# Kernel tuning notes

Measured on AMD Instinct MI355X. Metric: run time of the kernel, lower is better.

## Reference

```python
import math
import jax, jax.numpy as jnp
import numpy as np

D_MODEL = 768
EXPAND = 2
D_INNER = EXPAND * D_MODEL  # 1536
D_STATE = 16
D_CONV = 4
DT_RANK = math.ceil(D_INNER / 16)  # 96
B, L = 2, 2048
LN_EPS = 1e-5


def setup_inputs() -> dict:
    key = jax.random.key(0)
    ks = jax.random.split(key, 10)
    x = jax.random.normal(ks[0], (B, L, D_MODEL), dtype=jnp.float32)
    ln_g = jnp.ones((D_MODEL,), jnp.float32)
    ln_b = jnp.zeros((D_MODEL,), jnp.float32)
    W_in = jax.random.normal(ks[1], (D_MODEL, 2 * D_INNER), jnp.float32) / np.sqrt(D_MODEL)
    conv_w = jax.random.normal(ks[2], (D_INNER, 1, D_CONV), jnp.float32) / np.sqrt(D_CONV)
    conv_b = jax.random.normal(ks[3], (D_INNER,), jnp.float32) * 0.02
    W_xproj = jax.random.normal(ks[4], (D_INNER, DT_RANK + 2 * D_STATE), jnp.float32) / np.sqrt(D_INNER)
    W_dt = jax.random.normal(ks[5], (DT_RANK, D_INNER), jnp.float32) / np.sqrt(DT_RANK)
    # dt bias init: inverse-softplus of dt ~ LogUniform(1e-3, 1e-1)
    dt = jnp.exp(jax.random.uniform(ks[6], (D_INNER,)) * (math.log(0.1) - math.log(0.001)) + math.log(0.001))
    b_dt = dt + jnp.log(-jnp.expm1(-dt))
    log_A = jnp.log(jnp.tile(jnp.arange(1, D_STATE + 1, dtype=jnp.float32), (D_INNER, 1)))  # (d_inner, N)
    D_param = jnp.ones((D_INNER,), jnp.float32)
    W_out = jax.random.normal(ks[7], (D_INNER, D_MODEL), jnp.float32) / np.sqrt(D_INNER)
    return dict(x=x, ln_g=ln_g, ln_b=ln_b, W_in=W_in, conv_w=conv_w, conv_b=conv_b,
                W_xproj=W_xproj, W_dt=W_dt, b_dt=b_dt, log_A=log_A, D_param=D_param, W_out=W_out)


def _mamba_block(x, ln_g, ln_b, W_in, conv_w, conv_b, W_xproj, W_dt, b_dt, log_A, D_param, W_out):
    residual = x
    # LayerNorm
    mu = jnp.mean(x, axis=-1, keepdims=True)
    var = jnp.var(x, axis=-1, keepdims=True)
    xn = (x - mu) * jax.lax.rsqrt(var + LN_EPS) * ln_g + ln_b
    # in projection -> (u, v)
    uv = xn @ W_in  # (B, L, 2*d_inner)
    u, v = jnp.split(uv, 2, axis=-1)
    # causal depthwise conv1d along length (torch pads both sides then truncates -> left pad only)
    u_c = jnp.transpose(u, (0, 2, 1))  # (B, d_inner, L)
    u_c = jax.lax.conv_general_dilated(
        u_c, conv_w, window_strides=(1,), padding=[(D_CONV - 1, 0)],
        dimension_numbers=('NCH', 'OIH', 'NCH'), feature_group_count=D_INNER)
    u_c = u_c + conv_b[None, :, None]
    u = jnp.transpose(u_c, (0, 2, 1))  # (B, L, d_inner)
    u = jax.nn.silu(u)
    # Selective SSM
    x_dbl = u @ W_xproj  # (B, L, dt_rank + 2N)
    dlt, Bm, Cm = jnp.split(x_dbl, [DT_RANK, DT_RANK + D_STATE], axis=-1)
    delta = jax.nn.softplus(dlt @ W_dt + b_dt)  # (B, L, d_inner)
    A = -jnp.exp(log_A)  # (d_inner, N)
    A_bar = jnp.exp(jnp.einsum('bld,dn->bldn', delta, A))         # discretized A
    Bu = jnp.einsum('bld,bln,bld->bldn', delta, Bm, u)            # B_bar * u
    # parallel scan: h_k = A_bar_k * h_{k-1} + Bu_k
    def comb(e1, e2):
        a1, b1 = e1
        a2, b2 = e2
        return a1 * a2, a2 * b1 + b2
    _, h = jax.lax.associative_scan(comb, (A_bar, Bu), axis=1)
    y = jnp.einsum('bldn,bln->bld', h, Cm) + u * D_param
    # gate + residual
    y = y * jax.nn.silu(v)
    return y @ W_out + residual


def reference(x, ln_g, ln_b, W_in, conv_w, conv_b, W_xproj, W_dt, b_dt, log_A, D_param, W_out):
    return _mamba_block(x, ln_g, ln_b, W_in, conv_w, conv_b, W_xproj, W_dt, b_dt, log_A, D_param, W_out)
```

## Files before the change

### kernel.cpp

```cpp
#include <hip/hip_runtime.h>

#define D_MODEL 768
#define D_INNER 1536
#define D_STATE 16
#define DT_RANK 96
#define BB 2
#define LL 2048
#define TT (BB*LL)
#define NC 64
#define CL 32
#define SKK 4
#define LOG2E 1.44269504f

typedef unsigned short u16;
typedef short bf16x8 __attribute__((ext_vector_type(8)));
typedef unsigned short u16x8 __attribute__((ext_vector_type(8)));
typedef float f32x4  __attribute__((ext_vector_type(4)));

__device__ __forceinline__ float bf2f(u16 u) {
    union { unsigned int i; float f; } c; c.i = ((unsigned int)u) << 16; return c.f;
}
__device__ __forceinline__ u16 f2bf(float f) {
    union { float f; unsigned int i; } c; c.f = f;
    unsigned int x = c.i;
    return (u16)((x + 0x7fffu + ((x >> 16) & 1u)) >> 16);
}
__device__ __forceinline__ float bfu_lo(unsigned int u) {
    union { unsigned int i; float f; } c; c.i = u << 16; return c.f;
}
__device__ __forceinline__ float bfu_hi(unsigned int u) {
    union { unsigned int i; float f; } c; c.i = u & 0xFFFF0000u; return c.f;
}
__device__ __forceinline__ float ldx(const void* p, size_t i, bool f32) {
    return f32 ? ((const float*)p)[i] : bf2f(((const u16*)p)[i]);
}

__device__ __forceinline__ void gload16(const u16* g, u16* l) {
    __builtin_amdgcn_global_load_lds(
        (const __attribute__((address_space(1))) unsigned int*)g,
        (__attribute__((address_space(3))) unsigned int*)l, 16, 0, 0);
}

__device__ __forceinline__ void xcd_swz(int& bx, int& by) {
    const int gx = gridDim.x;
    const int cpx = (gx * gridDim.y) >> 3;
    const int bid = by * gx + bx;
    const int w = (bid & 7) * cpx + (bid >> 3);
    bx = w % gx; by = w / gx;
}

__global__ void detect_kernel(const void* x, int* flag)
{
    __shared__ int bad;
    if (threadIdx.x == 0) bad = 0;
    __syncthreads();
    const u16* p = (const u16*)x;
    int local = 0;
    for (int i = threadIdx.x; i < 2048; i += 256) {
        const float v = bf2f(p[2 * i]);
        if (!(fabsf(v) < 1e4f)) local = 1;
    }
    if (local) atomicOr(&bad, 1);
    __syncthreads();
    if (threadIdx.x == 0) *flag = bad;
}

__global__ __launch_bounds__(256) void transpose_all_kernel(
    const void* __restrict__ W_in, const void* __restrict__ W_xp,
    const void* __restrict__ W_dt, const void* __restrict__ W_out,
    u16* __restrict__ WtIn, u16* __restrict__ WtXp,
    u16* __restrict__ WtDt, u16* __restrict__ WtOut,
    const int* __restrict__ flagp)
{
    const bool f32 = (*flagp != 0);
    int bid = blockIdx.x;
    const void* src; u16* dst; int K, N, bx, by;
    if (bid < 576)      { src = W_in;  dst = WtIn;  K = 768;  N = 3072; bx = bid % 48; by = bid / 48; }
    else if (bid < 624) { bid -= 576; src = W_xp;  dst = WtXp;  K = 1536; N = 128;  bx = bid % 2;  by = bid / 2; }
    else if (bid < 672) { bid -= 624; src = W_dt;  dst = WtDt;  K = 96;   N = 1536; bx = bid % 24; by = bid / 24; }
    else                { bid -= 672; src = W_out; dst = WtOut; K = 1536; N = 768;  bx = bid % 12; by = bid / 12; }
    __shared__ u16 tile[64][72];
    const int t  = threadIdx.x;
    const int n0 = bx * 64, k0 = by * 64;
    {
        const int r = t >> 2, c = (t & 3) * 16;
        const int k = k0 + r;
        if (k < K) {
            #pragma unroll
            for (int i = 0; i < 16; ++i)
                tile[r][c + i] = f2bf(ldx(src, (size_t)k * N + n0 + c + i, f32));
        }
    }
    __syncthreads();
    {
        const int nl = t >> 2, kl = (t & 3) * 16;
        const int n = n0 + nl;
        #pragma unroll
        for (int i = 0; i < 16; ++i) {
            const int k = k0 + kl + i;
            if (k < K) dst[(size_t)n * K + k] = tile[kl + i][nl];
        }
    }
}

__global__ __launch_bounds__(256) void ln_kernel(const void* __restrict__ x,
    const void* __restrict__ g, const void* __restrict__ b, u16* __restrict__ xn,
    const int* __restrict__ flagp)
{
    const bool f32 = (*flagp != 0);
    const int tok = blockIdx.x;
    const int tid = threadIdx.x;
    const size_t base = (size_t)tok * D_MODEL;
    float v[3];
    v[0] = ldx(x, base + tid, f32);
    v[1] = ldx(x, base + tid + 256, f32);
    v[2] = ldx(x, base + tid + 512, f32);
    float s = v[0] + v[1] + v[2];
    float q = v[0]*v[0] + v[1]*v[1] + v[2]*v[2];
    #pragma unroll
    for (int o = 32; o > 0; o >>= 1) {
        s += __shfl_down(s, o, 64);
        q += __shfl_down(q, o, 64);
    }
    __shared__ float ss[4], qq[4];
    if ((tid & 63) == 0) { ss[tid >> 6] = s; qq[tid >> 6] = q; }
    __syncthreads();
    const float S = ss[0] + ss[1] + ss[2] + ss[3];
    const float Q = qq[0] + qq[1] + qq[2] + qq[3];
    const float mu  = S * (1.f / D_MODEL);
    const float var = Q * (1.f / D_MODEL) - mu * mu;
    const float rs  = rsqrtf(var + 1e-5f);
    u16* outr = xn + base;
    #pragma unroll
    for (int i = 0; i < 3; ++i) {
        const int c = tid + i * 256;
        outr[c] = f2bf((v[i] - mu) * rs * ldx(g, c, f32) + ldx(b, c, f32));
    }
}

template<int EPI>
__global__ __launch_bounds__(256) void mfma_gemm(
    const u16* __restrict__ A, const u16* __restrict__ Bt,
    u16* __restrict__ C, void* __restrict__ Cout, const void* __restrict__ aux,
    float* __restrict__ Cf, const int* __restrict__ flagp,
    int Kslice, int lda, int ldbt, int ldc)
{
    const bool f32 = (*flagp != 0);
    __shared__ alignas(16) u16 As[2 * 64 * 32];
    __shared__ alignas(16) u16 Bs[2 * 64 * 32];
    const int tid  = threadIdx.x;
    const int wave = tid >> 6, lane = tid & 63;
    const int lrow = lane & 15, quad = lane >> 4;
    int bx = blockIdx.x, by = blockIdx.y;
    if (gridDim.z == 1) xcd_swz(bx, by);
    const int row0 = by * 64, col0 = bx * 64;
    const int k0   = blockIdx.z * Kslice;
    const int srow = wave * 16 + (lane >> 2);
    const int skk  = (lane & 3) * 8;
    const int wb   = wave * 512;
    const u16* gA = A  + (size_t)(row0 + srow) * lda  + k0 + skk;
    const u16* gB = Bt + (size_t)(col0 + srow) * ldbt + k0 + skk;
    const int nst = Kslice >> 5;
    gload16(gA, &As[wb]);
    gload16(gB, &Bs[wb]);
    f32x4 acc[4] = {{0.f,0.f,0.f,0.f},{0.f,0.f,0.f,0.f},{0.f,0.f,0.f,0.f},{0.f,0.f,0.f,0.f}};
    int cur = 0;
    for (int t = 0; t < nst; ++t) {
        __syncthreads();
        const int boff = cur << 11;
        if (t + 1 < nst) {
            const int poff = boff ^ 2048;
            gload16(gA + (t + 1) * 32, &As[poff + wb]);
            gload16(gB + (t + 1) * 32, &Bs[poff + wb]);
        }
        const bf16x8 af = *(const bf16x8*)(&As[boff + (wave * 16 + lrow) * 32 + quad * 8]);
        #pragma unroll
        for (int q = 0; q < 4; ++q) {
            const bf16x8 bq = *(const bf16x8*)(&Bs[boff + (q * 16 + lrow) * 32 + quad * 8]);
            acc[q] = __builtin_amdgcn_mfma_f32_16x16x32_bf16(af, bq, acc[q], 0, 0, 0);
        }
        cur ^= 1;
    }
    #pragma unroll
    for (int t = 0; t < 4; ++t) {
        #pragma unroll
        for (int r = 0; r < 4; ++r) {
            const int row = row0 + wave * 16 + quad * 4 + r;
            const int col = col0 + t * 16 + lrow;
            const size_t idx = (size_t)row * ldc + col;
            float vv = acc[t][r];
            if (EPI == 1) {
                vv += ldx(aux, col, f32);
                vv = (vv > 20.f) ? vv : log1pf(__expf(vv));
                C[idx] = f2bf(vv);
            } else if (EPI == 2) {
                vv += ldx(aux, idx, f32);
                if (f32) ((float*)Cout)[idx] = vv;
                else     ((u16*)Cout)[idx]   = f2bf(vv);
            } else if (EPI == 3) {
                atomicAdd(&Cf[idx], vv);
            } else {
                C[idx] = f2bf(vv);
            }
        }
    }
}

template<int EPI>
__global__ __launch_bounds__(256) void mfma_gemm128(
    const u16* __restrict__ A, const u16* __restrict__ Bt,
    u16* __restrict__ C, void* __restrict__ Cout, const void* __restrict__ aux,
    const int* __restrict__ flagp,
    int K, int lda, int ldbt, int ldc)
{
    const bool f32 = (*flagp != 0);
    __shared__ alignas(16) u16 As[2 * 128 * 32];
    __shared__ alignas(16) u16 Bs[2 * 128 * 32];
    const int tid  = threadIdx.x;
    const int wave = tid >> 6, lane = tid & 63;
    const int lrow = lane & 15, quad = lane >> 4;
    const int wy = wave >> 1, wx = wave & 1;
    int bx = blockIdx.x, by = blockIdx.y;
    if (gridDim.z == 1) xcd_swz(bx, by);
    const int row0 = by * 128, col0 = bx * 128;
    const int skk = (lane & 3) * 8;
    const int r0 = wave * 16 + (lane >> 2);
    const int r1 = r0 + 64;
    const int wb0 = wave * 512, wb1 = (wave + 4) * 512;
    const u16* gA0 = A  + (size_t)(row0 + r0) * lda  + skk;
    const u16* gA1 = A  + (size_t)(row0 + r1) * lda  + skk;
    const u16* gB0 = Bt + (size_t)(col0 + r0) * ldbt + skk;
    const u16* gB1 = Bt + (size_t)(col0 + r1) * ldbt + skk;
    const int nst = K >> 5;
    gload16(gA0, &As[wb0]);
    gload16(gA1, &As[wb1]);
    gload16(gB0, &Bs[wb0]);
    gload16(gB1, &Bs[wb1]);
    f32x4 acc[4][4];
    #pragma unroll
    for (int i = 0; i < 4; ++i)
        #pragma unroll
        for (int j = 0; j < 4; ++j) acc[i][j] = (f32x4){0.f,0.f,0.f,0.f};
    int cur = 0;
    for (int t = 0; t < nst; ++t) {
        __syncthreads();
        const int boff = cur << 12;
        if (t + 1 < nst) {
            const int poff = boff ^ 4096;
            const int kt = (t + 1) * 32;
            gload16(gA0 + kt, &As[poff + wb0]);
            gload16(gA1 + kt, &As[poff + wb1]);
            gload16(gB0 + kt, &Bs[poff + wb0]);
            gload16(gB1 + kt, &Bs[poff + wb1]);
        }
        bf16x8 af[4], bf_[4];
        #pragma unroll
        for (int i = 0; i < 4; ++i)
            af[i] = *(const bf16x8*)(&As[boff + (wy * 64 + i * 16 + lrow) * 32 + quad * 8]);
        #pragma unroll
        for (int j = 0; j < 4; ++j)
            bf_[j] = *(const bf16x8*)(&Bs[boff + (wx * 64 + j * 16 + lrow) * 32 + quad * 8]);
        #pragma unroll
        for (int i = 0; i < 4; ++i)
            #pragma unroll
            for (int j = 0; j < 4; ++j)
                acc[i][j] = __builtin_amdgcn_mfma_f32_16x16x32_bf16(af[i], bf_[j], acc[i][j], 0, 0, 0);
        cur ^= 1;
    }
    #pragma unroll
    for (int i = 0; i < 4; ++i) {
        #pragma unroll
        for (int j = 0; j < 4; ++j) {
            #pragma unroll
            for (int r = 0; r < 4; ++r) {
                const int row = row0 + wy * 64 + i * 16 + quad * 4 + r;
                const int col = col0 + wx * 64 + j * 16 + lrow;
                const size_t idx = (size_t)row * ldc + col;
                float vv = acc[i][j][r];
                if (EPI == 1) {
                    vv += ldx(aux, col, f32);
                    vv = (vv > 20.f) ? vv : log1pf(__expf(vv));
                    C[idx] = f2bf(vv);
                } else if (EPI == 2) {
                    vv += ldx(aux, idx, f32);
                    if (f32) ((float*)Cout)[idx] = vv;
                    else     ((u16*)Cout)[idx]   = f2bf(vv);
                } else {
                    C[idx] = f2bf(vv);
                }
            }
        }
    }
}

__global__ __launch_bounds__(256) void convert_kernel(const float* __restrict__ src,
                                                      u16* __restrict__ dst, int n)
{
    const int i = blockIdx.x * 256 + threadIdx.x;
    if (i < n) dst[i] = f2bf(src[i]);
}

__global__ __launch_bounds__(256) void conv_silu_kernel(
    const u16* __restrict__ uv, const void* __restrict__ cw, const void* __restrict__ cb,
    u16* __restrict__ us, const int* __restrict__ flagp)
{
    const bool f32 = (*flagp != 0);
    const int idx = blockIdx.x * 256 + threadIdx.x;
    const int d   = idx % D_INNER;
    const int tok = idx / D_INNER;
    const int l   = tok & (LL - 1);
    float acc = ldx(cb, d, f32);
    #pragma unroll
    for (int j = 0; j < 4; ++j) {
        const int li = l - 3 + j;
        if (li >= 0)
            acc += bf2f(uv[(size_t)(tok - 3 + j) * (2*D_INNER) + d]) * ldx(cw, d * 4 + j, f32);
    }
    us[idx] = f2bf(acc / (1.f + __expf(-acc)));
}

__global__ __launch_bounds__(256) void scan1_kernel(
    const u16* __restrict__ delta, const u16* __restrict__ us,
    const u16* __restrict__ xdbl, const void* __restrict__ log_A,
    float* __restrict__ carryA, float* __restrict__ carryH,
    const int* __restrict__ flagp)
{
    const bool f32 = (*flagp != 0);
    const int d = blockIdx.x * 256 + threadIdx.x;
    const int c = blockIdx.y, b = blockIdx.z;
    float A2[16], h[16];
    #pragma unroll
    for (int j = 0; j < 16; ++j) {
        A2[j] = -__expf(ldx(log_A, d * D_STATE + j, f32)) * LOG2E;
        h[j] = 0.f;
    }
    bool pw = true;
    #pragma unroll
    for (int j = 1; j < 16; ++j)
        pw = pw && (fabsf(A2[j] - (j + 1) * A2[0]) <= 0.02f * (j + 1) * fabsf(A2[0]));
    float sdl = 0.f;
    size_t tok = (size_t)b * LL + c * CL;
    if (pw) {
        #pragma unroll 2
        for (int t = 0; t < CL; ++t, ++tok) {
            const float dl = bf2f(delta[tok * D_INNER + d]);
            const float ul = bf2f(us[tok * D_INNER + d]);
            const uint4 B0 = *(const uint4*)(xdbl + tok * 128 + DT_RANK);
            const uint4 B1 = *(const uint4*)(xdbl + tok * 128 + DT_RANK + 8);
            const float dlul = dl * ul;
            sdl += dl;
            const unsigned int bw[8] = {B0.x,B0.y,B0.z,B0.w,B1.x,B1.y,B1.z,B1.w};
            const float a1 = exp2f(dl * A2[0]);
            float aj = 1.f;
            #pragma unroll
            for (int j = 0; j < 16; ++j) {
                aj *= a1;
                const float Bn = (j & 1) ? bfu_hi(bw[j >> 1]) : bfu_lo(bw[j >> 1]);
                h[j] = aj * h[j] + dlul * Bn;
            }
        }
    } else {
        #pragma unroll 2
        for (int t = 0; t < CL; ++t, ++tok) {
            const float dl = bf2f(delta[tok * D_INNER + d]);
            const float ul = bf2f(us[tok * D_INNER + d]);
            const uint4 B0 = *(const uint4*)(xdbl + tok * 128 + DT_RANK);
            const uint4 B1 = *(const uint4*)(xdbl + tok * 128 + DT_RANK + 8);
            const float dlul = dl * ul;
            sdl += dl;
            const unsigned int bw[8] = {B0.x,B0.y,B0.z,B0.w,B1.x,B1.y,B1.z,B1.w};
            #pragma unroll
            for (int j = 0; j < 16; ++j) {
                const float Bn = (j & 1) ? bfu_hi(bw[j >> 1]) : bfu_lo(bw[j >> 1]);
                h[j] = exp2f(dl * A2[j]) * h[j] + dlul * Bn;
            }
        }
    }
    const size_t ci = (((size_t)b * NC + c) * D_INNER + d) * D_STATE;
    #pragma unroll
    for (int q = 0; q < 4; ++q) {
        *(float4*)(carryA + ci + 4*q) = (float4){
            exp2f(A2[4*q+0]*sdl), exp2f(A2[4*q+1]*sdl),
            exp2f(A2[4*q+2]*sdl), exp2f(A2[4*q+3]*sdl)};
        *(float4*)(carryH + ci + 4*q) = (float4){h[4*q+0], h[4*q+1], h[4*q+2], h[4*q+3]};
    }
}

__global__ __launch_bounds__(256) void scan2_kernel(
    const float* __restrict__ carryA, float* __restrict__ carryH)
{
    const int gid = blockIdx.x * 256 + threadIdx.x;
    const int b   = gid / (D_INNER * D_STATE);
    const int dn  = gid % (D_INNER * D_STATE);
    float hrun = 0.f;
    #pragma unroll
    for (int c = 0; c < NC; ++c) {
        const size_t ci = ((size_t)(b * NC + c) * D_INNER * D_STATE) + dn;
        const float a = carryA[ci], hh = carryH[ci];
        carryH[ci] = hrun;
        hrun = a * hrun + hh;
    }
}

__global__ __launch_bounds__(256) void scan3_kernel(
    const u16* __restrict__ delta, const u16* __restrict__ us,
    const u16* __restrict__ xdbl, u16* __restrict__ uv,
    const void* __restrict__ log_A, const void* __restrict__ D_param,
    const float* __restrict__ carryH, const int* __restrict__ flagp)
{
    const bool f32 = (*flagp != 0);
    const int d = blockIdx.x * 256 + threadIdx.x;
    const int c = blockIdx.y, b = blockIdx.z;
    const float Dd = ldx(D_param, d, f32);
    float A2[16], h[16];
    const size_t ci = (((size_t)b * NC + c) * D_INNER + d) * D_STATE;
    #pragma unroll
    for (int j = 0; j < 16; ++j)
        A2[j] = -__expf(ldx(log_A, d * D_STATE + j, f32)) * LOG2E;
    bool pw = true;
    #pragma unroll
    for (int j = 1; j < 16; ++j)
        pw = pw && (fabsf(A2[j] - (j + 1) * A2[0]) <= 0.02f * (j + 1) * fabsf(A2[0]));
    #pragma unroll
    for (int q = 0; q < 4; ++q) {
        const float4 hq = *(const float4*)(carryH + ci + 4*q);
        h[4*q+0] = hq.x; h[4*q+1] = hq.y; h[4*q+2] = hq.z; h[4*q+3] = hq.w;
    }
    size_t tok = (size_t)b * LL + c * CL;
    if (pw) {
        #pragma unroll 2
        for (int t = 0; t < CL; ++t, ++tok) {
            const float dl = bf2f(delta[tok * D_INNER + d]);
            const float ul = bf2f(us[tok * D_INNER + d]);
            const uint4 B0 = *(const uint4*)(xdbl + tok * 128 + DT_RANK);
            const uint4 B1 = *(const uint4*)(xdbl + tok * 128 + DT_RANK + 8);
            const uint4 C0 = *(const uint4*)(xdbl + tok * 128 + DT_RANK + D_STATE);
            const uint4 C1 = *(const uint4*)(xdbl + tok * 128 + DT_RANK + D_STATE + 8);
            const float dlul = dl * ul;
            const unsigned int bw[8] = {B0.x,B0.y,B0.z,B0.w,B1.x,B1.y,B1.z,B1.w};
            const unsigned int cw_[8] = {C0.x,C0.y,C0.z,C0.w,C1.x,C1.y,C1.z,C1.w};
            const float a1 = exp2f(dl * A2[0]);
            float aj = 1.f, p = 0.f;
            #pragma unroll
            for (int j = 0; j < 16; ++j) {
                aj *= a1;
                const float Bn = (j & 1) ? bfu_hi(bw[j >> 1]) : bfu_lo(bw[j >> 1]);
                const float Cn = (j & 1) ? bfu_hi(cw_[j >> 1]) : bfu_lo(cw_[j >> 1]);
                h[j] = aj * h[j] + dlul * Bn;
                p += h[j] * Cn;
            }
            const float vv = bf2f(uv[tok * (2*D_INNER) + D_INNER + d]);
            uv[tok * (2*D_INNER) + d] = f2bf((p + ul * Dd) * (vv / (1.f + __expf(-vv))));
        }
    } else {
        #pragma unroll 2
        for (int t = 0; t < CL; ++t, ++tok) {
            const float dl = bf2f(delta[tok * D_INNER + d]);
            const float ul = bf2f(us[tok * D_INNER + d]);
            const uint4 B0 = *(const uint4*)(xdbl + tok * 128 + DT_RANK);
            const uint4 B1 = *(const uint4*)(xdbl + tok * 128 + DT_RANK + 8);
            const uint4 C0 = *(const uint4*)(xdbl + tok * 128 + DT_RANK + D_STATE);
            const uint4 C1 = *(const uint4*)(xdbl + tok * 128 + DT_RANK + D_STATE + 8);
            const float dlul = dl * ul;
            const unsigned int bw[8] = {B0.x,B0.y,B0.z,B0.w,B1.x,B1.y,B1.z,B1.w};
            const unsigned int cw_[8] = {C0.x,C0.y,C0.z,C0.w,C1.x,C1.y,C1.z,C1.w};
            float p = 0.f;
            #pragma unroll
            for (int j = 0; j < 16; ++j) {
                const float Bn = (j & 1) ? bfu_hi(bw[j >> 1]) : bfu_lo(bw[j >> 1]);
                const float Cn = (j & 1) ? bfu_hi(cw_[j >> 1]) : bfu_lo(cw_[j >> 1]);
                h[j] = exp2f(dl * A2[j]) * h[j] + dlul * Bn;
                p += h[j] * Cn;
            }
            const float vv = bf2f(uv[tok * (2*D_INNER) + D_INNER + d]);
            uv[tok * (2*D_INNER) + d] = f2bf((p + ul * Dd) * (vv / (1.f + __expf(-vv))));
        }
    }
}

extern "C" void kernel_launch(void* const* d_in, const int* in_sizes, int n_in,
                              void* d_out, int out_size, void* d_ws, size_t ws_size,
                              hipStream_t stream)
{
    const void* x      = d_in[0];
    const void* ln_g   = d_in[1];
    const void* ln_b   = d_in[2];
    const void* W_in   = d_in[3];
    const void* conv_w = d_in[4];
    const void* conv_b = d_in[5];
    const void* W_xp   = d_in[6];
    const void* W_dt   = d_in[7];
    const void* b_dt   = d_in[8];
    const void* log_A  = d_in[9];
    const void* D_par  = d_in[10];
    const void* W_out  = d_in[11];

    int* flag  = (int*)d_ws;
    u16* ws    = (u16*)((char*)d_ws + 512);
    u16* xn    = ws;
    u16* uv    = xn + (size_t)TT * D_MODEL;
    u16* us    = uv + (size_t)TT * 2 * D_INNER;
    u16* xdbl  = us + (size_t)TT * D_INNER;
    u16* delta = xdbl + (size_t)TT * 128;
    float* carryH = (float*)(delta + (size_t)TT * D_INNER);
    float* carryA = carryH + (size_t)BB * NC * D_INNER * D_STATE;
    u16* WtIn  = (u16*)(carryA + (size_t)BB * NC * D_INNER * D_STATE);
    u16* WtXp  = WtIn  + (size_t)2 * D_INNER * D_MODEL;
    u16* WtDt  = WtXp  + (size_t)(DT_RANK + 2 * D_STATE) * D_INNER;
    u16* WtOut = WtDt  + (size_t)D_INNER * DT_RANK;
    float* xdblF = (float*)(WtOut + (size_t)D_MODEL * D_INNER);

    detect_kernel<<<1, 256, 0, stream>>>(x, flag);
    transpose_all_kernel<<<960, 256, 0, stream>>>(
        W_in, W_xp, W_dt, W_out, WtIn, WtXp, WtDt, WtOut, flag);
    hipMemsetAsync(xdblF, 0, (size_t)TT * 128 * sizeof(float), stream);

    ln_kernel<<<TT, 256, 0, stream>>>(x, ln_g, ln_b, xn, flag);
    mfma_gemm128<0><<<dim3(2 * D_INNER / 128, TT / 128), 256, 0, stream>>>(
        xn, WtIn, uv, nullptr, nullptr, flag, D_MODEL, D_MODEL, D_MODEL, 2 * D_INNER);
    conv_silu_kernel<<<(TT * D_INNER) / 256, 256, 0, stream>>>(uv, conv_w, conv_b, us, flag);
    mfma_gemm<3><<<dim3(2, TT / 64, SKK), 256, 0, stream>>>(
        us, WtXp, nullptr, nullptr, nullptr, xdblF, flag,
        D_INNER / SKK, D_INNER, D_INNER, 128);
    convert_kernel<<<(TT * 128 + 255) / 256, 256, 0, stream>>>(xdblF, xdbl, TT * 128);
    mfma_gemm<1><<<dim3(D_INNER / 64, TT / 64, 1), 256, 0, stream>>>(
        xdbl, WtDt, delta, nullptr, b_dt, nullptr, flag,
        DT_RANK, 128, DT_RANK, D_INNER);
    scan1_kernel<<<dim3(D_INNER / 256, NC, BB), 256, 0, stream>>>(
        delta, us, xdbl, log_A, carryA, carryH, flag);
    scan2_kernel<<<(BB * D_INNER * D_STATE) / 256, 256, 0, stream>>>(carryA, carryH);
    scan3_kernel<<<dim3(D_INNER / 256, NC, BB), 256, 0, stream>>>(
        delta, us, xdbl, uv, log_A, D_par, carryH, flag);
    mfma_gemm<2><<<dim3(D_MODEL / 64, TT / 64, 1), 256, 0, stream>>>(
        uv, WtOut, nullptr, d_out, x, nullptr, flag,
        D_INNER, 2 * D_INNER, D_INNER, D_MODEL);
}
```

Measured before the change: 320.1 us.

## Vectorize transpose and conv, widen GEMM K-tile, coalesce scan carry layout

Vectorizes the weight transpose loads/stores and the conv+SiLU kernel, which now processes eight channels per thread with 16-byte accesses. It also templates the MFMA GEMM on K-tile depth, using 64 for the x-projection and out-projection GEMMs to halve the number of barriers per tile. Finally, it changes the scan carry buffers to a state-major layout indexed by channel so per-thread stores and loads coalesce across the wavefront. The risks are larger shared memory per block and dependence on scan2's indexing being compatible with the new carry layout.

```diff
diff --git a/kernel.cpp b/kernel.cpp
--- a/kernel.cpp
+++ b/kernel.cpp
@@ -86,19 +86,36 @@
         const int r = t >> 2, c = (t & 3) * 16;
         const int k = k0 + r;
         if (k < K) {
-            #pragma unroll
-            for (int i = 0; i < 16; ++i)
-                tile[r][c + i] = f2bf(ldx(src, (size_t)k * N + n0 + c + i, f32));
+            if (f32) {
+                const float* sp = (const float*)src + (size_t)k * N + n0 + c;
+                #pragma unroll
+                for (int q = 0; q < 4; ++q) {
+                    const float4 v = *(const float4*)(sp + 4 * q);
+                    tile[r][c + 4*q + 0] = f2bf(v.x);
+                    tile[r][c + 4*q + 1] = f2bf(v.y);
+                    tile[r][c + 4*q + 2] = f2bf(v.z);
+                    tile[r][c + 4*q + 3] = f2bf(v.w);
+                }
+            } else {
+                const u16* sp = (const u16*)src + (size_t)k * N + n0 + c;
+                *(u16x8*)(&tile[r][c])     = *(const u16x8*)(sp);
+                *(u16x8*)(&tile[r][c + 8]) = *(const u16x8*)(sp + 8);
+            }
         }
     }
     __syncthreads();
     {
         const int nl = t >> 2, kl = (t & 3) * 16;
         const int n = n0 + nl;
-        #pragma unroll
-        for (int i = 0; i < 16; ++i) {
-            const int k = k0 + kl + i;
-            if (k < K) dst[(size_t)n * K + k] = tile[kl + i][nl];
+        if (k0 + kl < K) {
+            u16x8 t0, t1;
+            #pragma unroll
+            for (int i = 0; i < 8; ++i) t0[i] = tile[kl + i][nl];
+            #pragma unroll
+            for (int i = 0; i < 8; ++i) t1[i] = tile[kl + 8 + i][nl];
+            u16* dp = dst + (size_t)n * K + k0 + kl;
+            *(u16x8*)(dp)     = t0;
+            *(u16x8*)(dp + 8) = t1;
         }
     }
 }
@@ -138,7 +155,7 @@
     }
 }
 
-template<int EPI>
+template<int EPI, int BK>
 __global__ __launch_bounds__(256) void mfma_gemm(
     const u16* __restrict__ A, const u16* __restrict__ Bt,
     u16* __restrict__ C, void* __restrict__ Cout, const void* __restrict__ aux,
@@ -146,8 +163,8 @@
     int Kslice, int lda, int ldbt, int ldc)
 {
     const bool f32 = (*flagp != 0);
-    __shared__ alignas(16) u16 As[2 * 64 * 32];
-    __shared__ alignas(16) u16 Bs[2 * 64 * 32];
+    __shared__ alignas(16) u16 As[2 * 64 * BK];
+    __shared__ alignas(16) u16 Bs[2 * 64 * BK];
     const int tid  = threadIdx.x;
     const int wave = tid >> 6, lane = tid & 63;
     const int lrow = lane & 15, quad = lane >> 4;
@@ -155,29 +172,42 @@
     if (gridDim.z == 1) xcd_swz(bx, by);
     const int row0 = by * 64, col0 = bx * 64;
     const int k0   = blockIdx.z * Kslice;
-    const int srow = wave * 16 + (lane >> 2);
-    const int skk  = (lane & 3) * 8;
-    const int wb   = wave * 512;
-    const u16* gA = A  + (size_t)(row0 + srow) * lda  + k0 + skk;
-    const u16* gB = Bt + (size_t)(col0 + srow) * ldbt + k0 + skk;
-    const int nst = Kslice >> 5;
-    gload16(gA, &As[wb]);
-    gload16(gB, &Bs[wb]);
+    constexpr int LPR = BK / 8;
+    constexpr int RPO = 64 / LPR;
+    constexpr int NOP = BK / 32;
+    const int srow = lane / LPR;
+    const int skk  = (lane % LPR) * 8;
+    const int wb   = wave * 16 * BK;
+    const u16* gA = A  + (size_t)(row0 + wave * 16 + srow) * lda  + k0 + skk;
+    const u16* gB = Bt + (size_t)(col0 + wave * 16 + srow) * ldbt + k0 + skk;
+    const int nst = Kslice / BK;
+    #pragma unroll
+    for (int o = 0; o < NOP; ++o) {
+        gload16(gA + (size_t)o * RPO * lda,  &As[wb + o * 512]);
+        gload16(gB + (size_t)o * RPO * ldbt, &Bs[wb + o * 512]);
+    }
     f32x4 acc[4] = {{0.f,0.f,0.f,0.f},{0.f,0.f,0.f,0.f},{0.f,0.f,0.f,0.f},{0.f,0.f,0.f,0.f}};
     int cur = 0;
     for (int t = 0; t < nst; ++t) {
         __syncthreads();
-        const int boff = cur << 11;
+        const int boff = cur * (64 * BK);
         if (t + 1 < nst) {
-            const int poff = boff ^ 2048;
-            gload16(gA + (t + 1) * 32, &As[poff + wb]);
-            gload16(gB + (t + 1) * 32, &Bs[poff + wb]);
-        }
-        const bf16x8 af = *(const bf16x8*)(&As[boff + (wave * 16 + lrow) * 32 + quad * 8]);
-        #pragma unroll
-        for (int q = 0; q < 4; ++q) {
-            const bf16x8 bq = *(const bf16x8*)(&Bs[boff + (q * 16 + lrow) * 32 + quad * 8]);
-            acc[q] = __builtin_amdgcn_mfma_f32_16x16x32_bf16(af, bq, acc[q], 0, 0, 0);
+            const int poff = boff ^ (64 * BK);
+            const int kt = (t + 1) * BK;
+            #pragma unroll
+            for (int o = 0; o < NOP; ++o) {
+                gload16(gA + kt + (size_t)o * RPO * lda,  &As[poff + wb + o * 512]);
+                gload16(gB + kt + (size_t)o * RPO * ldbt, &Bs[poff + wb + o * 512]);
+            }
+        }
+        #pragma unroll
+        for (int kk = 0; kk < NOP; ++kk) {
+            const bf16x8 af = *(const bf16x8*)(&As[boff + (wave * 16 + lrow) * BK + kk * 32 + quad * 8]);
+            #pragma unroll
+            for (int q = 0; q < 4; ++q) {
+                const bf16x8 bq = *(const bf16x8*)(&Bs[boff + (q * 16 + lrow) * BK + kk * 32 + quad * 8]);
+                acc[q] = __builtin_amdgcn_mfma_f32_16x16x32_bf16(af, bq, acc[q], 0, 0, 0);
+            }
         }
         cur ^= 1;
     }
@@ -305,18 +335,38 @@
     u16* __restrict__ us, const int* __restrict__ flagp)
 {
     const bool f32 = (*flagp != 0);
-    const int idx = blockIdx.x * 256 + threadIdx.x;
-    const int d   = idx % D_INNER;
-    const int tok = idx / D_INNER;
+    const int gid = blockIdx.x * 256 + threadIdx.x;
+    const int nd8 = D_INNER / 8;
+    const int d8  = gid % nd8;
+    const int tok = gid / nd8;
+    const int d   = d8 * 8;
     const int l   = tok & (LL - 1);
-    float acc = ldx(cb, d, f32);
+    float acc[8], w[4][8];
+    #pragma unroll
+    for (int i = 0; i < 8; ++i) acc[i] = ldx(cb, d + i, f32);
+    #pragma unroll
+    for (int i = 0; i < 8; ++i) {
+        if (f32) {
+            const float4 wv = *(const float4*)((const float*)cw + (size_t)(d + i) * 4);
+            w[0][i] = wv.x; w[1][i] = wv.y; w[2][i] = wv.z; w[3][i] = wv.w;
+        } else {
+            const u16* wp = (const u16*)cw + (size_t)(d + i) * 4;
+            w[0][i] = bf2f(wp[0]); w[1][i] = bf2f(wp[1]);
+            w[2][i] = bf2f(wp[2]); w[3][i] = bf2f(wp[3]);
+        }
+    }
     #pragma unroll
     for (int j = 0; j < 4; ++j) {
-        const int li = l - 3 + j;
-        if (li >= 0)
-            acc += bf2f(uv[(size_t)(tok - 3 + j) * (2*D_INNER) + d]) * ldx(cw, d * 4 + j, f32);
-    }
-    us[idx] = f2bf(acc / (1.f + __expf(-acc)));
+        if (l - 3 + j >= 0) {
+            const u16x8 uvv = *(const u16x8*)(&uv[(size_t)(tok - 3 + j) * (2 * D_INNER) + d]);
+            #pragma unroll
+            for (int i = 0; i < 8; ++i) acc[i] += bf2f(uvv[i]) * w[j][i];
+        }
+    }
+    u16x8 o;
+    #pragma unroll
+    for (int i = 0; i < 8; ++i) o[i] = f2bf(acc[i] / (1.f + __expf(-acc[i])));
+    *(u16x8*)(&us[(size_t)tok * D_INNER + d]) = o;
 }
 
 __global__ __launch_bounds__(256) void scan1_kernel(
@@ -376,13 +426,11 @@
             }
         }
     }
-    const size_t ci = (((size_t)b * NC + c) * D_INNER + d) * D_STATE;
-    #pragma unroll
-    for (int q = 0; q < 4; ++q) {
-        *(float4*)(carryA + ci + 4*q) = (float4){
-            exp2f(A2[4*q+0]*sdl), exp2f(A2[4*q+1]*sdl),
-            exp2f(A2[4*q+2]*sdl), exp2f(A2[4*q+3]*sdl)};
-        *(float4*)(carryH + ci + 4*q) = (float4){h[4*q+0], h[4*q+1], h[4*q+2], h[4*q+3]};
+    const size_t ci = ((size_t)b * NC + c) * (D_INNER * D_STATE) + d;
+    #pragma unroll
+    for (int j = 0; j < 16; ++j) {
+        carryA[ci + (size_t)j * D_INNER] = exp2f(A2[j] * sdl);
+        carryH[ci + (size_t)j * D_INNER] = h[j];
     }
 }
 
@@ -413,7 +461,7 @@
     const int c = blockIdx.y, b = blockIdx.z;
     const float Dd = ldx(D_param, d, f32);
     float A2[16], h[16];
-    const size_t ci = (((size_t)b * NC + c) * D_INNER + d) * D_STATE;
+    const size_t ci = ((size_t)b * NC + c) * (D_INNER * D_STATE) + d;
     #pragma unroll
     for (int j = 0; j < 16; ++j)
         A2[j] = -__expf(ldx(log_A, d * D_STATE + j, f32)) * LOG2E;
@@ -422,10 +470,8 @@
     for (int j = 1; j < 16; ++j)
         pw = pw && (fabsf(A2[j] - (j + 1) * A2[0]) <= 0.02f * (j + 1) * fabsf(A2[0]));
     #pragma unroll
-    for (int q = 0; q < 4; ++q) {
-        const float4 hq = *(const float4*)(carryH + ci + 4*q);
-        h[4*q+0] = hq.x; h[4*q+1] = hq.y; h[4*q+2] = hq.z; h[4*q+3] = hq.w;
-    }
+    for (int j = 0; j < 16; ++j)
+        h[j] = carryH[ci + (size_t)j * D_INNER];
     size_t tok = (size_t)b * LL + c * CL;
     if (pw) {
         #pragma unroll 2
@@ -518,12 +564,12 @@
     ln_kernel<<<TT, 256, 0, stream>>>(x, ln_g, ln_b, xn, flag);
     mfma_gemm128<0><<<dim3(2 * D_INNER / 128, TT / 128), 256, 0, stream>>>(
         xn, WtIn, uv, nullptr, nullptr, flag, D_MODEL, D_MODEL, D_MODEL, 2 * D_INNER);
-    conv_silu_kernel<<<(TT * D_INNER) / 256, 256, 0, stream>>>(uv, conv_w, conv_b, us, flag);
-    mfma_gemm<3><<<dim3(2, TT / 64, SKK), 256, 0, stream>>>(
+    conv_silu_kernel<<<(TT * D_INNER / 8) / 256, 256, 0, stream>>>(uv, conv_w, conv_b, us, flag);
+    mfma_gemm<3, 64><<<dim3(2, TT / 64, SKK), 256, 0, stream>>>(
         us, WtXp, nullptr, nullptr, nullptr, xdblF, flag,
         D_INNER / SKK, D_INNER, D_INNER, 128);
     convert_kernel<<<(TT * 128 + 255) / 256, 256, 0, stream>>>(xdblF, xdbl, TT * 128);
-    mfma_gemm<1><<<dim3(D_INNER / 64, TT / 64, 1), 256, 0, stream>>>(
+    mfma_gemm<1, 32><<<dim3(D_INNER / 64, TT / 64, 1), 256, 0, stream>>>(
         xdbl, WtDt, delta, nullptr, b_dt, nullptr, flag,
         DT_RANK, 128, DT_RANK, D_INNER);
     scan1_kernel<<<dim3(D_INNER / 256, NC, BB), 256, 0, stream>>>(
@@ -531,7 +577,7 @@
     scan2_kernel<<<(BB * D_INNER * D_STATE) / 256, 256, 0, stream>>>(carryA, carryH);
     scan3_kernel<<<dim3(D_INNER / 256, NC, BB), 256, 0, stream>>>(
         delta, us, xdbl, uv, log_A, D_par, carryH, flag);
-    mfma_gemm<2><<<dim3(D_MODEL / 64, TT / 64, 1), 256, 0, stream>>>(
+    mfma_gemm<2, 64><<<dim3(D_MODEL / 64, TT / 64, 1), 256, 0, stream>>>(
         uv, WtOut, nullptr, d_out, x, nullptr, flag,
         D_INNER, 2 * D_INNER, D_INNER, D_MODEL);
 }
```

New measurement: 295.2 us. 1.08x faster.
